# Kernel optimization log

Hardware: AMD Instinct MI355X
Metric: run time of the kernel (lower is better)

## Reference

```python
import jax, jax.numpy as jnp
import numpy as np

NUM_ADDRESSES = 100000
ADDRESS_DIM = 1024
CONTENT_DIM = 1024
BATCH = 512
THRESHOLD = 110  # address_dim - 2*binom.ppf(p=0.000368, n=1024, 0.5)


def setup_inputs() -> dict:
    key = jax.random.key(0)
    k1, k2, k3 = jax.random.split(key, 3)
    # bipolar (+1/-1) hypervectors, as produced by torchhd.functional.random (MAP)
    address = jnp.sign(jax.random.normal(k1, (BATCH, ADDRESS_DIM), dtype=jnp.float32))
    addresses = jnp.sign(jax.random.normal(k2, (NUM_ADDRESSES, ADDRESS_DIM), dtype=jnp.float32))
    # content counters (functional.empty is arbitrary; use gaussian values)
    content = jax.random.normal(k3, (NUM_ADDRESSES, CONTENT_DIM), dtype=jnp.float32)
    return {"address": address, "addresses": addresses, "content": content,
            "threshold": THRESHOLD}


def reference(address, addresses, content, threshold):
    # dot_similarity for MAP tensors is a plain inner product: [B, N]
    similarity = jnp.einsum("bd,nd->bn", address, addresses)
    is_active = similarity >= threshold  # [B, N] boolean
    # Equivalent of nonzero + index_add scatter into per-row accumulators:
    # sum content rows of all active addresses for each query.
    read = jnp.einsum("bn,nc->bc", is_active.astype(address.dtype), content)
    return jnp.sign(read)
```

## Files before the change

kernel.cpp:

```cpp
#include <hip/hip_runtime.h>
#include <stdint.h>

#define DIM    1024
#define NQ     512
#define CAP    512
#define RPB    64
#define KC     128
#define NCHUNK (DIM / KC)


typedef __attribute__((ext_vector_type(8))) short bf16x8;
typedef __attribute__((ext_vector_type(4))) float f32x4;

__global__ __launch_bounds__(256) void k0_pack(const float* __restrict__ address,
                                               uint32_t* __restrict__ qbf,
                                               int* __restrict__ cnt) {
  const int g = blockIdx.x * 256 + threadIdx.x;
  const float4 v = reinterpret_cast<const float4*>(address)[g];
  uint2 u;
  u.x = (__float_as_uint(v.x) >> 16) | (__float_as_uint(v.y) & 0xFFFF0000u);
  u.y = (__float_as_uint(v.z) >> 16) | (__float_as_uint(v.w) & 0xFFFF0000u);
  reinterpret_cast<uint2*>(qbf)[g] = u;
  if (g < NQ) cnt[g] = 0;
}

__global__ __launch_bounds__(512) void k1_sim(const float* __restrict__ addresses,
                                              const uint32_t* __restrict__ qbf,
                                              const void* __restrict__ thr_raw,
                                              int* __restrict__ cnt,
                                              uint32_t* __restrict__ buckets,
                                              int N) {
  __shared__ uint32_t blds[RPB * KC / 2];
  const int t    = threadIdx.x;
  const int base = blockIdx.x * RPB;

  int thr;
  {
    const int ti = *reinterpret_cast<const int*>(thr_raw);
    if (ti >= -DIM && ti <= DIM) thr = ti;
    else {
      const float tf = *reinterpret_cast<const float*>(thr_raw);
      thr = (int)floorf(tf + 0.5f);
    }
  }
  const float thrf = (float)thr;

  const int w     = t >> 6;
  const int l     = t & 63;
  const int l16   = l & 15;
  const int lk    = l >> 4;
  const int qrow0 = w * 64;

  const int sr   = t >> 3;
  const int sc   = t & 7;
  const int krow = base + sr;

  f32x4 acc[4][4];
#pragma unroll
  for (int mt = 0; mt < 4; ++mt)
#pragma unroll
    for (int nt = 0; nt < 4; ++nt)
      acc[mt][nt] = (f32x4){0.f, 0.f, 0.f, 0.f};

  float4 stg[4];
#define LOAD_CHUNK(KCI)                                                              \
  _Pragma("unroll") for (int j = 0; j < 4; ++j) {                                    \
    const int fi = sc + 8 * j;                                                       \
    if (krow < N)                                                                    \
      stg[j] = *reinterpret_cast<const float4*>(                                     \
          addresses + (size_t)krow * DIM + (KCI) * KC + fi * 4);                     \
    else                                                                             \
      stg[j] = make_float4(0.f, 0.f, 0.f, 0.f);                                      \
  }

  LOAD_CHUNK(0);

#pragma unroll 1
  for (int kc = 0; kc < NCHUNK; ++kc) {
#pragma unroll
    for (int j = 0; j < 4; ++j) {
      const int fi = sc + 8 * j;
      uint2 u;
      u.x = (__float_as_uint(stg[j].x) >> 16) | (__float_as_uint(stg[j].y) & 0xFFFF0000u);
      u.y = (__float_as_uint(stg[j].z) >> 16) | (__float_as_uint(stg[j].w) & 0xFFFF0000u);
      const int lbyte = (sr * 256 + fi * 8) ^ ((sr & 7) << 4);
      *reinterpret_cast<uint2*>(reinterpret_cast<char*>(blds) + lbyte) = u;
    }
    __syncthreads();

    if (kc + 1 < NCHUNK) LOAD_CHUNK(kc + 1);

#pragma unroll
    for (int ks = 0; ks < 4; ++ks) {
      bf16x8 a[4], b[4];
      const int kglob = kc * KC + ks * 32 + lk * 8;
#pragma unroll
      for (int mt = 0; mt < 4; ++mt) {
        const int q = qrow0 + mt * 16 + l16;
        a[mt] = *reinterpret_cast<const bf16x8*>(
            reinterpret_cast<const char*>(qbf) + ((size_t)q * DIM + kglob) * 2);
      }
#pragma unroll
      for (int nt = 0; nt < 4; ++nt) {
        const int n = nt * 16 + l16;
        const int lbyte = (n * 256 + (ks * 32 + lk * 8) * 2) ^ ((n & 7) << 4);
        b[nt] = *reinterpret_cast<const bf16x8*>(
            reinterpret_cast<const char*>(blds) + lbyte);
      }
#pragma unroll
      for (int mt = 0; mt < 4; ++mt)
#pragma unroll
        for (int nt = 0; nt < 4; ++nt)
          acc[mt][nt] = __builtin_amdgcn_mfma_f32_16x16x32_bf16(
              a[mt], b[nt], acc[mt][nt], 0, 0, 0);
    }
    __syncthreads();
  }
#undef LOAD_CHUNK

#pragma unroll
  for (int mt = 0; mt < 4; ++mt) {
#pragma unroll
    for (int nt = 0; nt < 4; ++nt) {
      const int n = base + nt * 16 + l16;
#pragma unroll
      for (int r = 0; r < 4; ++r) {
        const float s = acc[mt][nt][r];
        if (s >= thrf && n < N) {
          const int q   = qrow0 + mt * 16 + lk * 4 + r;
          const int idx = atomicAdd(&cnt[q], 1);
          if (idx < CAP) buckets[(size_t)q * CAP + idx] = (uint32_t)n;
        }
      }
    }
  }
}

__global__ __launch_bounds__(256) void k2_gather(const float* __restrict__ content,
                                                 const int* __restrict__ cnt,
                                                 const uint32_t* __restrict__ buckets,
                                                 float* __restrict__ out) {
  __shared__ uint32_t list[CAP];
  const int b = blockIdx.x;
  const int t = threadIdx.x;
  int c = cnt[b];
  if (c > CAP) c = CAP;
  for (int i = t; i < c; i += 256) list[i] = buckets[(size_t)b * CAP + i];
  __syncthreads();

  double a0 = 0, a1 = 0, a2 = 0, a3 = 0;
  const float4* __restrict__ c4 = reinterpret_cast<const float4*>(content);
  for (int i = 0; i < c; ++i) {
    const float4 v = c4[(size_t)list[i] * (DIM / 4) + t];
    a0 += v.x; a1 += v.y; a2 += v.z; a3 += v.w;
  }
  float4 r;
  r.x = a0 > 0.0 ? 1.0f : (a0 < 0.0 ? -1.0f : 0.0f);
  r.y = a1 > 0.0 ? 1.0f : (a1 < 0.0 ? -1.0f : 0.0f);
  r.z = a2 > 0.0 ? 1.0f : (a2 < 0.0 ? -1.0f : 0.0f);
  r.w = a3 > 0.0 ? 1.0f : (a3 < 0.0 ? -1.0f : 0.0f);
  reinterpret_cast<float4*>(out)[(size_t)b * (DIM / 4) + t] = r;
}

extern "C" void kernel_launch(void* const* d_in, const int* in_sizes, int n_in,
                              void* d_out, int out_size, void* d_ws, size_t ws_size,
                              hipStream_t stream) {
  const float* address   = (const float*)d_in[0];
  const float* addresses = (const float*)d_in[1];
  const float* content   = (const float*)d_in[2];
  const void*  thr       = d_in[3];
  const int N = in_sizes[1] / DIM;

  char* ws = (char*)d_ws;
  int*      cnt     = (int*)ws;
  uint32_t* qbf     = (uint32_t*)(ws + 2048);
  uint32_t* buckets = (uint32_t*)(ws + 2048 + NQ * DIM * 2);

  k0_pack<<<512, 256, 0, stream>>>(address, qbf, cnt);
  const int nb = (N + RPB - 1) / RPB;
  k1_sim<<<nb, 512, 0, stream>>>(addresses, qbf, thr, cnt, buckets, N);
  k2_gather<<<NQ, 256, 0, stream>>>(content, cnt, buckets, (float*)d_out);
}
```

Measured before the change: 889.9 us.

## Convert sign vectors to FP8 in a pre-pass and tile similarity GEMM over queries

Adds a conversion kernel that packs the address matrix into swizzled FP8 bytes holding exact ±1. The similarity kernel now uses a 2D grid of 128x128 query×address tiles, stages them through double-buffered LDS with direct global-to-LDS loads, and runs FP8 MFMA instead of BF16. Operand bytes drop fourfold for the GEMM and the query tile is shared through LDS rather than read from global memory per wave. In exchange there is an extra full pass over the 400MB fp32 address matrix plus a 100MB write, and the address tile is now reread for each of the four query tiles.

```diff
diff --git a/kernel.cpp b/kernel.cpp
--- a/kernel.cpp
+++ b/kernel.cpp
@@ -4,130 +4,138 @@
 #define DIM    1024
 #define NQ     512
 #define CAP    512
-#define RPB    64
-#define KC     128
-#define NCHUNK (DIM / KC)
+#define QT     128
+#define NT     128
+#define BK     128
+#define KSTEPS (DIM/BK)
+#define NTILES 782
+#define NPAD   (NTILES*NT)
 
 
-typedef __attribute__((ext_vector_type(8))) short bf16x8;
 typedef __attribute__((ext_vector_type(4))) float f32x4;
 
-__global__ __launch_bounds__(256) void k0_pack(const float* __restrict__ address,
-                                               uint32_t* __restrict__ qbf,
-                                               int* __restrict__ cnt) {
+__device__ __forceinline__ uint32_t pack4(const float4 v) {
+  return ( ((__float_as_uint(v.x) >> 31 << 7) | 0x38u)       )
+       | ( ((__float_as_uint(v.y) >> 31 << 7) | 0x38u) <<  8 )
+       | ( ((__float_as_uint(v.z) >> 31 << 7) | 0x38u) << 16 )
+       | ( ((__float_as_uint(v.w) >> 31 << 7) | 0x38u) << 24 );
+}
+
+__global__ __launch_bounds__(256) void k0_queries(const float* __restrict__ address,
+                                                  uint8_t* __restrict__ qf8,
+                                                  int* __restrict__ cnt) {
   const int g = blockIdx.x * 256 + threadIdx.x;
-  const float4 v = reinterpret_cast<const float4*>(address)[g];
-  uint2 u;
-  u.x = (__float_as_uint(v.x) >> 16) | (__float_as_uint(v.y) & 0xFFFF0000u);
-  u.y = (__float_as_uint(v.z) >> 16) | (__float_as_uint(v.w) & 0xFFFF0000u);
-  reinterpret_cast<uint2*>(qbf)[g] = u;
+  const int n = g >> 6, d0 = (g & 63) * 16;
+  const float4* src = reinterpret_cast<const float4*>(address + (size_t)n * DIM + d0);
+  uint4 o;
+  o.x = pack4(src[0]); o.y = pack4(src[1]); o.z = pack4(src[2]); o.w = pack4(src[3]);
+  *reinterpret_cast<uint4*>(qf8 + (size_t)n * DIM + (d0 ^ ((n & 7) << 4))) = o;
   if (g < NQ) cnt[g] = 0;
 }
 
-__global__ __launch_bounds__(512) void k1_sim(const float* __restrict__ addresses,
-                                              const uint32_t* __restrict__ qbf,
-                                              const void* __restrict__ thr_raw,
-                                              int* __restrict__ cnt,
-                                              uint32_t* __restrict__ buckets,
-                                              int N) {
-  __shared__ uint32_t blds[RPB * KC / 2];
-  const int t    = threadIdx.x;
-  const int base = blockIdx.x * RPB;
+__global__ __launch_bounds__(256) void k1a_convert(const float* __restrict__ addresses,
+                                                   uint8_t* __restrict__ abf8,
+                                                   int N) {
+  const int g = blockIdx.x * 256 + threadIdx.x;
+  const int n = g >> 6, d0 = (g & 63) * 16;
+  uint4 o = make_uint4(0u, 0u, 0u, 0u);
+  if (n < N) {
+    const float4* src = reinterpret_cast<const float4*>(addresses + (size_t)n * DIM + d0);
+    o.x = pack4(src[0]); o.y = pack4(src[1]); o.z = pack4(src[2]); o.w = pack4(src[3]);
+  }
+  *reinterpret_cast<uint4*>(abf8 + (size_t)n * DIM + (d0 ^ ((n & 7) << 4))) = o;
+}
+
+__global__ __launch_bounds__(256, 2) void k1_sim(const uint8_t* __restrict__ abf8,
+                                                 const uint8_t* __restrict__ qf8,
+                                                 const void* __restrict__ thr_raw,
+                                                 int* __restrict__ cnt,
+                                                 uint32_t* __restrict__ buckets,
+                                                 int N) {
+  __shared__ __align__(16) uint8_t lds[2][2][QT * BK];
+  const int t  = threadIdx.x;
+  const int qt = blockIdx.x;
+  const int nt = blockIdx.y;
+  const int w  = t >> 6, l = t & 63;
 
   int thr;
   {
     const int ti = *reinterpret_cast<const int*>(thr_raw);
     if (ti >= -DIM && ti <= DIM) thr = ti;
-    else {
-      const float tf = *reinterpret_cast<const float*>(thr_raw);
-      thr = (int)floorf(tf + 0.5f);
-    }
+    else thr = (int)floorf(*reinterpret_cast<const float*>(thr_raw) + 0.5f);
   }
   const float thrf = (float)thr;
 
-  const int w     = t >> 6;
-  const int l     = t & 63;
-  const int l16   = l & 15;
-  const int lk    = l >> 4;
-  const int qrow0 = w * 64;
+  const uint8_t* __restrict__ Abase = qf8  + (size_t)(qt * QT) * DIM;
+  const uint8_t* __restrict__ Bbase = abf8 + (size_t)(nt * NT) * DIM;
 
-  const int sr   = t >> 3;
-  const int sc   = t & 7;
-  const int krow = base + sr;
+  auto stage = [&](int buf, int s) {
+#pragma unroll
+    for (int i = 0; i < 4; ++i) {
+      const int D = w * 4096 + i * 1024 + l * 16;
+      const int r = D >> 7;
+      const int c = D & 127;
+      __builtin_amdgcn_global_load_lds(
+          (const __attribute__((address_space(1))) void*)(Abase + (size_t)r * DIM + s * BK + c),
+          (__attribute__((address_space(3))) void*)(&lds[buf][0][D]), 16, 0, 0);
+      __builtin_amdgcn_global_load_lds(
+          (const __attribute__((address_space(1))) void*)(Bbase + (size_t)r * DIM + s * BK + c),
+          (__attribute__((address_space(3))) void*)(&lds[buf][1][D]), 16, 0, 0);
+    }
+  };
 
   f32x4 acc[4][4];
 #pragma unroll
   for (int mt = 0; mt < 4; ++mt)
 #pragma unroll
-    for (int nt = 0; nt < 4; ++nt)
-      acc[mt][nt] = (f32x4){0.f, 0.f, 0.f, 0.f};
+    for (int ntt = 0; ntt < 4; ++ntt)
+      acc[mt][ntt] = (f32x4){0.f, 0.f, 0.f, 0.f};
 
-  float4 stg[4];
-#define LOAD_CHUNK(KCI)                                                              \
-  _Pragma("unroll") for (int j = 0; j < 4; ++j) {                                    \
-    const int fi = sc + 8 * j;                                                       \
-    if (krow < N)                                                                    \
-      stg[j] = *reinterpret_cast<const float4*>(                                     \
-          addresses + (size_t)krow * DIM + (KCI) * KC + fi * 4);                     \
-    else                                                                             \
-      stg[j] = make_float4(0.f, 0.f, 0.f, 0.f);                                      \
-  }
+  const int wr   = (w >> 1) * 64;
+  const int wc   = (w & 1) * 64;
+  const int l15  = l & 15;
+  const int swz  = (l & 7) << 4;
+  const int goct = (l >> 4) * 8;
 
-  LOAD_CHUNK(0);
-
+  stage(0, 0);
+  int cur = 0;
 #pragma unroll 1
-  for (int kc = 0; kc < NCHUNK; ++kc) {
-#pragma unroll
-    for (int j = 0; j < 4; ++j) {
-      const int fi = sc + 8 * j;
-      uint2 u;
-      u.x = (__float_as_uint(stg[j].x) >> 16) | (__float_as_uint(stg[j].y) & 0xFFFF0000u);
-      u.y = (__float_as_uint(stg[j].z) >> 16) | (__float_as_uint(stg[j].w) & 0xFFFF0000u);
-      const int lbyte = (sr * 256 + fi * 8) ^ ((sr & 7) << 4);
-      *reinterpret_cast<uint2*>(reinterpret_cast<char*>(blds) + lbyte) = u;
-    }
+  for (int s = 0; s < KSTEPS; ++s) {
     __syncthreads();
-
-    if (kc + 1 < NCHUNK) LOAD_CHUNK(kc + 1);
-
+    if (s + 1 < KSTEPS) stage(cur ^ 1, s + 1);
+    const uint8_t* __restrict__ A = lds[cur][0];
+    const uint8_t* __restrict__ B = lds[cur][1];
 #pragma unroll
     for (int ks = 0; ks < 4; ++ks) {
-      bf16x8 a[4], b[4];
-      const int kglob = kc * KC + ks * 32 + lk * 8;
+      const int cbase = (ks * 32 + goct) ^ swz;
+      long a[4], b[4];
 #pragma unroll
-      for (int mt = 0; mt < 4; ++mt) {
-        const int q = qrow0 + mt * 16 + l16;
-        a[mt] = *reinterpret_cast<const bf16x8*>(
-            reinterpret_cast<const char*>(qbf) + ((size_t)q * DIM + kglob) * 2);
-      }
+      for (int mt = 0; mt < 4; ++mt)
+        a[mt] = *reinterpret_cast<const long*>(A + (wr + mt * 16 + l15) * BK + cbase);
 #pragma unroll
-      for (int nt = 0; nt < 4; ++nt) {
-        const int n = nt * 16 + l16;
-        const int lbyte = (n * 256 + (ks * 32 + lk * 8) * 2) ^ ((n & 7) << 4);
-        b[nt] = *reinterpret_cast<const bf16x8*>(
-            reinterpret_cast<const char*>(blds) + lbyte);
-      }
+      for (int ntt = 0; ntt < 4; ++ntt)
+        b[ntt] = *reinterpret_cast<const long*>(B + (wc + ntt * 16 + l15) * BK + cbase);
 #pragma unroll
       for (int mt = 0; mt < 4; ++mt)
 #pragma unroll
-        for (int nt = 0; nt < 4; ++nt)
-          acc[mt][nt] = __builtin_amdgcn_mfma_f32_16x16x32_bf16(
-              a[mt], b[nt], acc[mt][nt], 0, 0, 0);
+        for (int ntt = 0; ntt < 4; ++ntt)
+          acc[mt][ntt] = __builtin_amdgcn_mfma_f32_16x16x32_fp8_fp8(
+              a[mt], b[ntt], acc[mt][ntt], 0, 0, 0);
     }
-    __syncthreads();
+    cur ^= 1;
   }
-#undef LOAD_CHUNK
 
+  const int nb = nt * NT + wc;
+  const int qb = qt * QT + wr + (l >> 4) * 4;
 #pragma unroll
   for (int mt = 0; mt < 4; ++mt) {
 #pragma unroll
-    for (int nt = 0; nt < 4; ++nt) {
-      const int n = base + nt * 16 + l16;
+    for (int ntt = 0; ntt < 4; ++ntt) {
+      const int n = nb + ntt * 16 + l15;
 #pragma unroll
       for (int r = 0; r < 4; ++r) {
-        const float s = acc[mt][nt][r];
-        if (s >= thrf && n < N) {
-          const int q   = qrow0 + mt * 16 + lk * 4 + r;
+        if (acc[mt][ntt][r] >= thrf && n < N) {
+          const int q   = qb + mt * 16 + r;
           const int idx = atomicAdd(&cnt[q], 1);
           if (idx < CAP) buckets[(size_t)q * CAP + idx] = (uint32_t)n;
         }
@@ -173,11 +181,12 @@
 
   char* ws = (char*)d_ws;
   int*      cnt     = (int*)ws;
-  uint32_t* qbf     = (uint32_t*)(ws + 2048);
-  uint32_t* buckets = (uint32_t*)(ws + 2048 + NQ * DIM * 2);
+  uint8_t*  qf8     = (uint8_t*)(ws + 2048);
+  uint32_t* buckets = (uint32_t*)(ws + 526336);
+  uint8_t*  abf8    = (uint8_t*)(ws + 1574912);
 
-  k0_pack<<<512, 256, 0, stream>>>(address, qbf, cnt);
-  const int nb = (N + RPB - 1) / RPB;
-  k1_sim<<<nb, 512, 0, stream>>>(addresses, qbf, thr, cnt, buckets, N);
+  k0_queries<<<128, 256, 0, stream>>>(address, qf8, cnt);
+  k1a_convert<<<(NPAD * 64) / 256, 256, 0, stream>>>(addresses, abf8, N);
+  k1_sim<<<dim3(4, NTILES), 256, 0, stream>>>(abf8, qf8, thr, cnt, buckets, N);
   k2_gather<<<NQ, 256, 0, stream>>>(content, cnt, buckets, (float*)d_out);
 }
```

Result: faster. 794.9 us (-10.7%).
